# Performance work log

Measured on AMD Instinct MI355X. Metric: run time of the kernel, lower is better.

## Reference

```python
import jax, jax.numpy as jnp
import numpy as np

TAU = 0.5

def setup_inputs() -> dict:
    key = jax.random.key(0)
    ks = jax.random.split(key, 9)
    B, N, C, T, R = 32, 196, 768, 10, 16
    s = 0.02
    return {
        "x": jax.random.normal(ks[0], (B, N, C), jnp.float32),
        "W_qkv": jax.random.normal(ks[1], (3 * C, C), jnp.float32) * s,
        "b_qkv": jax.random.normal(ks[2], (3 * C,), jnp.float32) * s,
        "A_q": jax.random.normal(ks[3], (T, R, C), jnp.float32) * s,
        "B_q": jax.random.normal(ks[4], (T, C, R), jnp.float32) * s,
        "A_v": jax.random.normal(ks[5], (T, R, C), jnp.float32) * s,
        "B_v": jax.random.normal(ks[6], (T, C, R), jnp.float32) * s,
        "gate_logits_q": jax.random.normal(ks[7], (T,), jnp.float32),
        "gate_logits_v": jax.random.normal(ks[8], (T,), jnp.float32),
    }

def _fro(w):
    # Frobenius norm per task: w is [T, d1, d2]
    return jnp.sqrt(jnp.sum(w * w, axis=(1, 2)))

def _lora_branch(x, A, B, logits):
    # x: [B,N,C]; A: [T,R,C]; B: [T,C,R]; logits: [T]
    gate = jax.nn.softmax(logits / TAU)                      # soft gumbel gate, eval (no noise)
    scale = gate / (_fro(A) * _fro(B))                       # fuse 1/(||A||*||B||) with gate weight
    tmp = jnp.einsum('bnc,trc->tbnr', x, A)                  # low-rank projections, all tasks batched
    return jnp.einsum('tbnr,tcr,t->bnc', tmp, B, scale)      # up-project + weighted sum over tasks

def reference(x, W_qkv, b_qkv, A_q, B_q, A_v, B_v, gate_logits_q, gate_logits_v):
    C = x.shape[-1]
    qkv = jnp.einsum('bnc,dc->bnd', x, W_qkv) + b_qkv        # [B,N,3C]
    new_q = _lora_branch(x, A_q, B_q, gate_logits_q)
    new_v = _lora_branch(x, A_v, B_v, gate_logits_v)
    qkv = qkv.at[:, :, :C].add(new_q)
    qkv = qkv.at[:, :, 2 * C:].add(new_v)
    return qkv
```

## Files before the change

### kernel.cpp

```cpp
#include <hip/hip_runtime.h>

#define TAU_INV 2.0f

typedef unsigned short u16;
typedef short bf16x8 __attribute__((ext_vector_type(8)));
typedef float f32x4 __attribute__((ext_vector_type(4)));
typedef u16 u16x4v __attribute__((ext_vector_type(4)));
typedef u16 u16x8v __attribute__((ext_vector_type(8)));

typedef __attribute__((address_space(1))) const void GASV;
typedef __attribute__((address_space(3))) void LASV;
#define GLOAD16(gp, lp) __builtin_amdgcn_global_load_lds((GASV*)(gp), (LASV*)(lp), 16, 0, 0)

__device__ __forceinline__ u16 f2bf(float f) {
  unsigned u = __float_as_uint(f);
  u += 0x7FFFu + ((u >> 16) & 1u);
  return (u16)(u >> 16);
}

__global__ __launch_bounds__(256) void k_scales(
    const float* __restrict__ Aq, const float* __restrict__ Bq,
    const float* __restrict__ Av, const float* __restrict__ Bv,
    const float* __restrict__ lq, const float* __restrict__ lv,
    float* __restrict__ scales) {
  const int br = blockIdx.x / 10, t = blockIdx.x % 10;
  const float* __restrict__ A = br ? Av : Aq;
  const float* __restrict__ B = br ? Bv : Bq;
  const float* __restrict__ lg = br ? lv : lq;
  const int tid = threadIdx.x;
  const float4* A4 = (const float4*)(A + t * 12288);
  const float4* B4 = (const float4*)(B + t * 12288);
  float sA = 0.f, sB = 0.f;
  for (int i = tid; i < 3072; i += 256) {
    float4 a = A4[i];
    float4 b = B4[i];
    sA += a.x * a.x + a.y * a.y + a.z * a.z + a.w * a.w;
    sB += b.x * b.x + b.y * b.y + b.z * b.z + b.w * b.w;
  }
  for (int off = 32; off; off >>= 1) {
    sA += __shfl_down(sA, off);
    sB += __shfl_down(sB, off);
  }
  __shared__ float rA[4], rB[4];
  if ((tid & 63) == 0) { rA[tid >> 6] = sA; rB[tid >> 6] = sB; }
  __syncthreads();
  if (tid == 0) {
    sA = rA[0] + rA[1] + rA[2] + rA[3];
    sB = rB[0] + rB[1] + rB[2] + rB[3];
    float mx = -1e30f;
    for (int j = 0; j < 10; ++j) mx = fmaxf(mx, lg[j] * TAU_INV);
    float den = 0.f, num = 0.f;
    for (int j = 0; j < 10; ++j) {
      float e = __expf(lg[j] * TAU_INV - mx);
      den += e;
      if (j == t) num = e;
    }
    scales[br * 16 + t] = (num / den) * rsqrtf(sA) * rsqrtf(sB);
  }
}

__global__ __launch_bounds__(256) void k_fuse(
    const float* __restrict__ x, u16* __restrict__ xb,
    const float* __restrict__ Aq, const float* __restrict__ Bq,
    const float* __restrict__ Av, const float* __restrict__ Bv,
    const float* __restrict__ W, const float* __restrict__ scales,
    u16* __restrict__ Weff) {
  const int bid = blockIdx.x;
  const int tid = threadIdx.x;
  if (bid < 2352) {
    const int i = (bid * 256 + tid) * 8;
    float4 v0 = *(const float4*)(x + i);
    float4 v1 = *(const float4*)(x + i + 4);
    u16x8v o;
    o[0] = f2bf(v0.x); o[1] = f2bf(v0.y); o[2] = f2bf(v0.z); o[3] = f2bf(v0.w);
    o[4] = f2bf(v1.x); o[5] = f2bf(v1.y); o[6] = f2bf(v1.z); o[7] = f2bf(v1.w);
    *(u16x8v*)(xb + i) = o;
    return;
  }
  if (bid < 2388) {
    const int base = 589824 + (bid - 2352) * 16384;
#pragma unroll
    for (int it = 0; it < 8; ++it) {
      const int i = base + (it * 256 + tid) * 8;
      float4 v0 = *(const float4*)(W + i);
      float4 v1 = *(const float4*)(W + i + 4);
      u16x8v o;
      o[0] = f2bf(v0.x); o[1] = f2bf(v0.y); o[2] = f2bf(v0.z); o[3] = f2bf(v0.w);
      o[4] = f2bf(v1.x); o[5] = f2bf(v1.y); o[6] = f2bf(v1.z); o[7] = f2bf(v1.w);
      *(u16x8v*)(Weff + i) = o;
    }
    return;
  }
  const int db = bid - 2388;
  const int br = db / 36, t36 = db % 36;
  const int tm = t36 / 6, tn = t36 % 6;
  const float* __restrict__ A = br ? Av : Aq;
  const float* __restrict__ B = br ? Bv : Bq;
  const int d0 = tm * 128, c0 = tn * 128;
  const int rowbase = br ? 1536 : 0;
  __shared__ u16 As[128 * 32];
  __shared__ u16 Bs[128 * 32];
  const int lane = tid & 63, w = tid >> 6, wm = w >> 1, wn = w & 1;
  const int lr = lane & 15, kb = lane >> 4;
  f32x4 acc[4][4];
#pragma unroll
  for (int i = 0; i < 4; ++i)
#pragma unroll
    for (int j = 0; j < 4; ++j)
#pragma unroll
      for (int e = 0; e < 4; ++e) acc[i][j][e] = 0.f;

  for (int it = 0; it < 5; ++it) {
    const int k0 = it * 32;
    if (it) __syncthreads();
#pragma unroll
    for (int i = 0; i < 4; ++i) {
      int q = tid + i * 256;
      int d = q >> 3;
      int k = (q & 7) * 4;
      int kg = k0 + k;
      int t = kg >> 4, r = kg & 15;
      float4 v = *(const float4*)(B + (t * 768 + d0 + d) * 16 + r);
      float s = scales[br * 16 + t];
      u16x4v o;
      o[0] = f2bf(v.x * s); o[1] = f2bf(v.y * s);
      o[2] = f2bf(v.z * s); o[3] = f2bf(v.w * s);
      *(u16x4v*)(As + q * 4) = o;
    }
#pragma unroll
    for (int i = 0; i < 4; ++i) {
      int q = tid + i * 256;
      int c = (q & 31) * 4;
      int kk = q >> 5;
      float4 v = *(const float4*)(A + (k0 + kk) * 768 + c0 + c);
      Bs[(c + 0) * 32 + kk] = f2bf(v.x);
      Bs[(c + 1) * 32 + kk] = f2bf(v.y);
      Bs[(c + 2) * 32 + kk] = f2bf(v.z);
      Bs[(c + 3) * 32 + kk] = f2bf(v.w);
    }
    __syncthreads();
    bf16x8 a[4], b[4];
#pragma unroll
    for (int i = 0; i < 4; ++i)
      a[i] = *(const bf16x8*)(As + (wm * 64 + i * 16 + lr) * 32 + kb * 8);
#pragma unroll
    for (int j = 0; j < 4; ++j)
      b[j] = *(const bf16x8*)(Bs + (wn * 64 + j * 16 + lr) * 32 + kb * 8);
#pragma unroll
    for (int i = 0; i < 4; ++i)
#pragma unroll
      for (int j = 0; j < 4; ++j)
        acc[i][j] = __builtin_amdgcn_mfma_f32_16x16x32_bf16(a[i], b[j], acc[i][j], 0, 0, 0);
  }
#pragma unroll
  for (int i = 0; i < 4; ++i)
#pragma unroll
    for (int jn = 0; jn < 4; ++jn)
#pragma unroll
      for (int j = 0; j < 4; ++j) {
        int row = rowbase + d0 + wm * 64 + i * 16 + kb * 4 + j;
        int col = c0 + wn * 64 + jn * 16 + lr;
        int g = row * 768 + col;
        Weff[g] = f2bf(W[g] + acc[i][jn][j]);
      }
}

__global__ __launch_bounds__(512, 2) void k_gemm(
    const u16* __restrict__ Xb,
    const u16* __restrict__ Wb,
    const float* __restrict__ bias,
    float* __restrict__ out) {
  const int b = blockIdx.x;
  const int xcd = b & 7, sub = b >> 3;
  const int wgid = (xcd == 0) ? sub : (29 + (xcd - 1) * 28 + sub);
  const int tn = wgid % 9, tm = wgid / 9;
  const int m0 = tm * 256, n0 = tn * 256;
  __shared__ char lds[131072];
  const int tid = threadIdx.x;
  const int lane = tid & 63;
  const int w = tid >> 6, wm = w >> 2, wn = w & 3;
  const int lr = lane & 15, kb = lane >> 4;
  const int cs0 = ((kb ^ (lr & 7)) << 4);
  const int cs1 = (((4 + kb) ^ (lr & 7)) << 4);
  const int arow = (wm * 128 + lr) << 7;
  const int brow = (wn * 64 + lr) << 7;
  const int r0 = tid >> 3;
  const int cb0 = (((tid & 7) ^ (r0 & 7)) << 3);
  const u16* pA = Xb + (m0 + r0) * 768 + cb0;
  const u16* pB = Wb + (n0 + r0) * 768 + cb0;
  const int wb = (tid >> 6) << 10;

  f32x4 acc[8][4];
#pragma unroll
  for (int i = 0; i < 8; ++i)
#pragma unroll
    for (int j = 0; j < 4; ++j)
#pragma unroll
      for (int e = 0; e < 4; ++e) acc[i][j][e] = 0.f;

#define STG_A(buf, kt, h)                                                        \
  {                                                                              \
    GLOAD16(pA + ((h)*128 + 0) * 768 + (kt)*64, lds + (buf)*32768 + (h)*16384 + 0 + wb);    \
    GLOAD16(pA + ((h)*128 + 64) * 768 + (kt)*64, lds + (buf)*32768 + (h)*16384 + 8192 + wb);\
  }
#define STG_B(buf, kt, h)                                                        \
  {                                                                              \
    GLOAD16(pB + ((h)*128 + 0) * 768 + (kt)*64, lds + 65536 + (buf)*32768 + (h)*16384 + 0 + wb);    \
    GLOAD16(pB + ((h)*128 + 64) * 768 + (kt)*64, lds + 65536 + (buf)*32768 + (h)*16384 + 8192 + wb);\
  }
#define LDA8(buf, mh)                                                            \
  {                                                                              \
    const char* p_ = lds + (buf)*32768 + arow + (mh)*8192;                       \
    a[0] = *(const bf16x8*)(p_ + 0 * 2048 + cs0);                                \
    a[1] = *(const bf16x8*)(p_ + 0 * 2048 + cs1);                                \
    a[2] = *(const bf16x8*)(p_ + 1 * 2048 + cs0);                                \
    a[3] = *(const bf16x8*)(p_ + 1 * 2048 + cs1);                                \
    a[4] = *(const bf16x8*)(p_ + 2 * 2048 + cs0);                                \
    a[5] = *(const bf16x8*)(p_ + 2 * 2048 + cs1);                                \
    a[6] = *(const bf16x8*)(p_ + 3 * 2048 + cs0);                                \
    a[7] = *(const bf16x8*)(p_ + 3 * 2048 + cs1);                                \
  }
#define LDB4(dst, buf, nh)                                                       \
  {                                                                              \
    const char* p_ = lds + 65536 + (buf)*32768 + brow + (nh)*4096;               \
    dst[0] = *(const bf16x8*)(p_ + 0 * 2048 + cs0);                              \
    dst[1] = *(const bf16x8*)(p_ + 0 * 2048 + cs1);                              \
    dst[2] = *(const bf16x8*)(p_ + 1 * 2048 + cs0);                              \
    dst[3] = *(const bf16x8*)(p_ + 1 * 2048 + cs1);                              \
  }
#define BAR()                          \
  {                                    \
    asm volatile("" ::: "memory");     \
    __builtin_amdgcn_s_barrier();      \
    asm volatile("" ::: "memory");     \
  }
#define MMQ(QM, QN, BREG)                                                        \
  {                                                                              \
    __builtin_amdgcn_s_setprio(1);                                               \
    _Pragma("unroll") for (int mf = 0; mf < 4; ++mf)                             \
        _Pragma("unroll") for (int nf = 0; nf < 2; ++nf)                         \
            _Pragma("unroll") for (int ks = 0; ks < 2; ++ks)                     \
                acc[(QM)*4 + mf][(QN)*2 + nf] =                                  \
        __builtin_amdgcn_mfma_f32_16x16x32_bf16(                                 \
            a[mf * 2 + ks], BREG[nf * 2 + ks], acc[(QM)*4 + mf][(QN)*2 + nf],    \
            0, 0, 0);                                                            \
    __builtin_amdgcn_s_setprio(0);                                               \
  }

  bf16x8 a[8], b0[4], b1[4];
  STG_A(0, 0, 0) STG_B(0, 0, 0) STG_A(0, 0, 1) STG_B(0, 0, 1)
  STG_A(1, 1, 0) STG_B(1, 1, 0) STG_A(1, 1, 1) STG_B(1, 1, 1)

#pragma unroll 1
  for (int kt = 0; kt < 12; ++kt) {
    const int cur = kt & 1;
    if (kt < 11) {
      asm volatile("s_waitcnt vmcnt(8)" ::: "memory");
    } else {
      asm volatile("s_waitcnt vmcnt(0)" ::: "memory");
    }
    BAR();
    LDA8(cur, 0)
    LDB4(b0, cur, 0)
    BAR();
    MMQ(0, 0, b0)
    BAR();
    LDB4(b1, cur, 1)
    BAR();
    MMQ(0, 1, b1)
    BAR();
    LDA8(cur, 1)
    if (kt < 10) { STG_B(cur, kt + 2, 0) STG_B(cur, kt + 2, 1) }
    BAR();
    MMQ(1, 1, b1)
    BAR();
    if (kt < 10) { STG_A(cur, kt + 2, 0) }
    BAR();
    MMQ(1, 0, b0)
    BAR();
    if (kt < 10) { STG_A(cur, kt + 2, 1) }
  }
#undef STG_A
#undef STG_B
#undef LDA8
#undef LDB4
#undef MMQ

  float br[4];
#pragma unroll
  for (int q = 0; q < 4; ++q)
    br[q] = bias[n0 + wn * 64 + (q >> 1) * 32 + (q & 1) * 16 + lr];
#pragma unroll
  for (int mh = 0; mh < 2; ++mh)
#pragma unroll
    for (int mf = 0; mf < 4; ++mf)
#pragma unroll
      for (int q = 0; q < 4; ++q)
#pragma unroll
        for (int e = 0; e < 4; ++e) {
          int m = m0 + wm * 128 + mh * 64 + mf * 16 + kb * 4 + e;
          int n = n0 + wn * 64 + (q >> 1) * 32 + (q & 1) * 16 + lr;
          if (m < 6272) out[m * 2304 + n] = acc[mh * 4 + mf][q][e] + br[q];
        }
}

extern "C" void kernel_launch(void* const* d_in, const int* in_sizes, int n_in,
                              void* d_out, int out_size, void* d_ws, size_t ws_size,
                              hipStream_t stream) {
  const float* x    = (const float*)d_in[0];
  const float* Wq   = (const float*)d_in[1];
  const float* bqkv = (const float*)d_in[2];
  const float* Aq   = (const float*)d_in[3];
  const float* Bq   = (const float*)d_in[4];
  const float* Av   = (const float*)d_in[5];
  const float* Bv   = (const float*)d_in[6];
  const float* lq   = (const float*)d_in[7];
  const float* lv   = (const float*)d_in[8];
  float* out = (float*)d_out;

  char* ws = (char*)d_ws;
  float* scales = (float*)ws;
  u16* xb   = (u16*)(ws + 256);
  u16* weff = (u16*)(ws + 256 + 9830400);

  k_scales<<<20, 256, 0, stream>>>(Aq, Bq, Av, Bv, lq, lv, scales);
  k_fuse<<<2460, 256, 0, stream>>>(x, xb, Aq, Bq, Av, Bv, Wq, scales, weff);
  k_gemm<<<225, 512, 0, stream>>>(xb, weff, bqkv, out);
}
```

Measured before the change: 175.8 us.

## Split fused prep kernel into LoRA-delta kernel with full-K LDS staging and x-cast kernel

Splits the combined prep kernel into two launches: one computes the scaled LoRA delta plus the W middle-block cast, the other casts x to bf16 with four chunks per thread. The delta kernel now stages all of K=160 into padded LDS tiles once, instead of looping with a sync per 32-wide K step. This removes four barrier/reload rounds per tile and gives the x cast its own wide grid. The cost is an extra kernel launch and much larger LDS use per block (about 84KB), which limits residency.

```diff
diff --git a/kernel.cpp b/kernel.cpp
--- a/kernel.cpp
+++ b/kernel.cpp
@@ -59,26 +59,17 @@
   }
 }
 
-__global__ __launch_bounds__(256) void k_fuse(
-    const float* __restrict__ x, u16* __restrict__ xb,
+__global__ __launch_bounds__(256) void k_dwmid(
     const float* __restrict__ Aq, const float* __restrict__ Bq,
     const float* __restrict__ Av, const float* __restrict__ Bv,
     const float* __restrict__ W, const float* __restrict__ scales,
     u16* __restrict__ Weff) {
+  __shared__ u16 As[128 * 168];
+  __shared__ u16 Bs[128 * 168];
   const int bid = blockIdx.x;
   const int tid = threadIdx.x;
-  if (bid < 2352) {
-    const int i = (bid * 256 + tid) * 8;
-    float4 v0 = *(const float4*)(x + i);
-    float4 v1 = *(const float4*)(x + i + 4);
-    u16x8v o;
-    o[0] = f2bf(v0.x); o[1] = f2bf(v0.y); o[2] = f2bf(v0.z); o[3] = f2bf(v0.w);
-    o[4] = f2bf(v1.x); o[5] = f2bf(v1.y); o[6] = f2bf(v1.z); o[7] = f2bf(v1.w);
-    *(u16x8v*)(xb + i) = o;
-    return;
-  }
-  if (bid < 2388) {
-    const int base = 589824 + (bid - 2352) * 16384;
+  if (bid >= 72) {
+    const int base = 589824 + (bid - 72) * 16384;
 #pragma unroll
     for (int it = 0; it < 8; ++it) {
       const int i = base + (it * 256 + tid) * 8;
@@ -91,17 +82,39 @@
     }
     return;
   }
-  const int db = bid - 2388;
-  const int br = db / 36, t36 = db % 36;
+  const int br = bid / 36, t36 = bid % 36;
   const int tm = t36 / 6, tn = t36 % 6;
   const float* __restrict__ A = br ? Av : Aq;
   const float* __restrict__ B = br ? Bv : Bq;
   const int d0 = tm * 128, c0 = tn * 128;
   const int rowbase = br ? 1536 : 0;
-  __shared__ u16 As[128 * 32];
-  __shared__ u16 Bs[128 * 32];
   const int lane = tid & 63, w = tid >> 6, wm = w >> 1, wn = w & 1;
   const int lr = lane & 15, kb = lane >> 4;
+
+  for (int j = 0; j < 20; ++j) {
+    int f = j * 256 + tid;
+    int d = f / 40;
+    int k = (f % 40) * 4;
+    int t = k >> 4, r = k & 15;
+    float4 v = *(const float4*)(B + (t * 768 + d0 + d) * 16 + r);
+    float s = scales[br * 16 + t];
+    u16x4v o;
+    o[0] = f2bf(v.x * s); o[1] = f2bf(v.y * s);
+    o[2] = f2bf(v.z * s); o[3] = f2bf(v.w * s);
+    *(u16x4v*)(As + d * 168 + k) = o;
+  }
+  for (int j = 0; j < 20; ++j) {
+    int f = j * 256 + tid;
+    int k = f / 32;
+    int c = (f % 32) * 4;
+    float4 v = *(const float4*)(A + k * 768 + c0 + c);
+    Bs[(c + 0) * 168 + k] = f2bf(v.x);
+    Bs[(c + 1) * 168 + k] = f2bf(v.y);
+    Bs[(c + 2) * 168 + k] = f2bf(v.z);
+    Bs[(c + 3) * 168 + k] = f2bf(v.w);
+  }
+  __syncthreads();
+
   f32x4 acc[4][4];
 #pragma unroll
   for (int i = 0; i < 4; ++i)
@@ -110,42 +123,15 @@
 #pragma unroll
       for (int e = 0; e < 4; ++e) acc[i][j][e] = 0.f;
 
-  for (int it = 0; it < 5; ++it) {
-    const int k0 = it * 32;
-    if (it) __syncthreads();
-#pragma unroll
-    for (int i = 0; i < 4; ++i) {
-      int q = tid + i * 256;
-      int d = q >> 3;
-      int k = (q & 7) * 4;
-      int kg = k0 + k;
-      int t = kg >> 4, r = kg & 15;
-      float4 v = *(const float4*)(B + (t * 768 + d0 + d) * 16 + r);
-      float s = scales[br * 16 + t];
-      u16x4v o;
-      o[0] = f2bf(v.x * s); o[1] = f2bf(v.y * s);
-      o[2] = f2bf(v.z * s); o[3] = f2bf(v.w * s);
-      *(u16x4v*)(As + q * 4) = o;
-    }
-#pragma unroll
-    for (int i = 0; i < 4; ++i) {
-      int q = tid + i * 256;
-      int c = (q & 31) * 4;
-      int kk = q >> 5;
-      float4 v = *(const float4*)(A + (k0 + kk) * 768 + c0 + c);
-      Bs[(c + 0) * 32 + kk] = f2bf(v.x);
-      Bs[(c + 1) * 32 + kk] = f2bf(v.y);
-      Bs[(c + 2) * 32 + kk] = f2bf(v.z);
-      Bs[(c + 3) * 32 + kk] = f2bf(v.w);
-    }
-    __syncthreads();
+#pragma unroll
+  for (int kt = 0; kt < 5; ++kt) {
     bf16x8 a[4], b[4];
 #pragma unroll
     for (int i = 0; i < 4; ++i)
-      a[i] = *(const bf16x8*)(As + (wm * 64 + i * 16 + lr) * 32 + kb * 8);
+      a[i] = *(const bf16x8*)(As + (wm * 64 + i * 16 + lr) * 168 + kt * 32 + kb * 8);
 #pragma unroll
     for (int j = 0; j < 4; ++j)
-      b[j] = *(const bf16x8*)(Bs + (wn * 64 + j * 16 + lr) * 32 + kb * 8);
+      b[j] = *(const bf16x8*)(Bs + (wn * 64 + j * 16 + lr) * 168 + kt * 32 + kb * 8);
 #pragma unroll
     for (int i = 0; i < 4; ++i)
 #pragma unroll
@@ -163,6 +149,20 @@
         int g = row * 768 + col;
         Weff[g] = f2bf(W[g] + acc[i][jn][j]);
       }
+}
+
+__global__ __launch_bounds__(256) void k_cast(const float* __restrict__ x,
+                                              u16* __restrict__ xb) {
+#pragma unroll
+  for (int it = 0; it < 4; ++it) {
+    const int i = ((blockIdx.x * 4 + it) * 256 + threadIdx.x) * 8;
+    float4 v0 = *(const float4*)(x + i);
+    float4 v1 = *(const float4*)(x + i + 4);
+    u16x8v o;
+    o[0] = f2bf(v0.x); o[1] = f2bf(v0.y); o[2] = f2bf(v0.z); o[3] = f2bf(v0.w);
+    o[4] = f2bf(v1.x); o[5] = f2bf(v1.y); o[6] = f2bf(v1.z); o[7] = f2bf(v1.w);
+    *(u16x8v*)(xb + i) = o;
+  }
 }
 
 __global__ __launch_bounds__(512, 2) void k_gemm(
@@ -324,6 +324,7 @@
   u16* weff = (u16*)(ws + 256 + 9830400);
 
   k_scales<<<20, 256, 0, stream>>>(Aq, Bq, Av, Bv, lq, lv, scales);
-  k_fuse<<<2460, 256, 0, stream>>>(x, xb, Aq, Bq, Av, Bv, Wq, scales, weff);
+  k_dwmid<<<108, 256, 0, stream>>>(Aq, Bq, Av, Bv, Wq, scales, weff);
+  k_cast<<<588, 256, 0, stream>>>(x, xb);
   k_gemm<<<225, 512, 0, stream>>>(xb, weff, bqkv, out);
 }
```

New measurement: 155.4 us. 1.13x faster.
